# Kernel optimization log

Hardware: AMD Instinct MI355X
Metric: run time of the kernel (lower is better)

Reference implementation:

```python
import jax, jax.numpy as jnp
import numpy as np

B, D = 128, 512
ORDER, DEPTH = 1, 2


def setup_inputs() -> dict:
    key = jax.random.key(0)
    kx, kw = jax.random.split(key)
    x = jax.random.normal(kx, (B, D), dtype=jnp.float32)
    # scale the cubic meta-weight so repeated contractions stay O(1)
    W = jax.random.normal(kw, (D, D, D), dtype=jnp.float32) * (1.0 / np.sqrt(D))
    bias = jnp.zeros((D,), dtype=jnp.float32)
    return {"x": x, "W": W, "bias": bias}


def reference(x, W, bias):
    # Meta-linear: per-sample effective weight obtained by contracting the
    # trailing `ORDER` modes of W (out, in, in, ...) with x, rescaled by
    # 1/sqrt(d) per contraction, then applied as a linear layer; repeat DEPTH times.
    sqrt_d = np.sqrt(x.shape[-1]).astype(np.float32)
    for _ in range(DEPTH):
        # first contraction introduces the batch dim: (out, in, k) x (b, k) -> (b, out, in)
        w = jnp.einsum('...k,bk->b...', W, x) / sqrt_d
        for _ in range(ORDER - 1):
            w = jnp.einsum('b...k,bk->b...', w, x) / sqrt_d
        x = jnp.einsum('boi,bi->bo', w, x) + bias
    return x
```

## Files before the change

kernel.cpp:

```cpp
#include <hip/hip_runtime.h>
#include <hip/hip_fp16.h>


typedef __attribute__((ext_vector_type(8))) _Float16 f16x8;
typedef __attribute__((ext_vector_type(4))) float    f32x4v;
typedef __attribute__((ext_vector_type(4))) unsigned u32x4;

#define DD 512
#define BB 128
#define INV_SQRT_D 0.04419417382415922f

static __device__ __forceinline__ unsigned pkh(float a, float b) {
    __half2 h = __float22half2_rn(make_float2(a, b));
    unsigned u; __builtin_memcpy(&u, &h, sizeof(u)); return u;
}
static __device__ __forceinline__ u32x4 pack8(f32x4v a, f32x4v b) {
    u32x4 r; r.x = pkh(a.x, a.y); r.y = pkh(a.z, a.w);
             r.z = pkh(b.x, b.y); r.w = pkh(b.z, b.w); return r;
}
static __device__ __forceinline__ f16x8 as_h8(u32x4 q) {
    f16x8 v; __builtin_memcpy(&v, &q, sizeof(v)); return v;
}

__global__ __launch_bounds__(256, 4)
void metagemm(const float* __restrict__ x, const float* __restrict__ W,
              float* __restrict__ part) {
    __shared__ u32x4    kp_lds[1024];
    __shared__ unsigned sc_lds[4096];

    const int tid  = threadIdx.x;
    const int lane = tid & 63;
    const int wv   = tid >> 6;
    const int bid  = blockIdx.x;
    const int ob   = bid >> 7;
    const int ig   = (bid >> 3) & 15;
    const int kp   = bid & 7;

    const int o0   = ob * 64 + wv * 16;
    const int i0   = ig * 32;
    const int kb   = kp * 64;
    const int l15  = lane & 15;
    const int quad = lane >> 4;
    const int koff = quad * 8;

    const float* wbase = W + (long)(o0 + l15) * (DD * DD) + (long)i0 * DD + kb + koff;

    f32x4v wa = *(const f32x4v*)(wbase);
    f32x4v wb = *(const f32x4v*)(wbase + 4);
    f32x4v wc = *(const f32x4v*)(wbase + 32);
    f32x4v wd = *(const f32x4v*)(wbase + 36);

#pragma unroll
    for (int ff = 0; ff < 2; ++ff) {
        const int f   = wv * 2 + ff;
        const int row = f * 16 + l15;
        const float* xr = x + row * DD + kb + koff;
#pragma unroll
        for (int ks = 0; ks < 2; ++ks) {
            f32x4v a = *(const f32x4v*)(xr + ks * 32);
            f32x4v b = *(const f32x4v*)(xr + ks * 32 + 4);
            kp_lds[(ks * 8 + f) * 64 + lane] = pack8(a, b);
        }
    }
    {
        const int row  = tid & 127;
        const int half = tid >> 7;
#pragma unroll
        for (int c4 = 0; c4 < 4; ++c4) {
            const int i = half * 16 + c4 * 4;
            f32x4v v = *(const f32x4v*)(x + row * DD + i0 + i);
#pragma unroll
            for (int j = 0; j < 4; ++j) {
                float s = v[j] * INV_SQRT_D;
                sc_lds[(i + j) * 128 + row] = pkh(s, s);
            }
        }
    }
    __syncthreads();

    f32x4v c[8];
#pragma unroll
    for (int f = 0; f < 8; ++f) c[f] = (f32x4v){0.f, 0.f, 0.f, 0.f};

    unsigned lic = 0;
#pragma unroll 1
    for (int n = 0; n < 32; ++n) {
        asm volatile("" : "+v"(lic));

        f32x4v ca = wa, cb = wb, cc = wc, cd = wd;
        if (n < 31) {
            const float* wp = wbase + (n + 1) * DD;
            wa = *(const f32x4v*)(wp);
            wb = *(const f32x4v*)(wp + 4);
            wc = *(const f32x4v*)(wp + 32);
            wd = *(const f32x4v*)(wp + 36);
        }

        f16x8 bf0 = as_h8(pack8(ca, cb));
        f16x8 bf1 = as_h8(pack8(cc, cd));

        const unsigned* scp = sc_lds + n * 128 + l15 + lic;
        const u32x4*    kpp = kp_lds + lane + lic;

#pragma unroll
        for (int f = 0; f < 8; ++f) {
            unsigned su = scp[f * 16];
            u32x4 sq = {su, su, su, su};
            f16x8 sv = as_h8(sq);
            f16x8 a0 = as_h8(kpp[f * 64]) * sv;
            c[f] = __builtin_amdgcn_mfma_f32_16x16x32_f16(a0, bf0, c[f], 0, 0, 0);
            f16x8 a1 = as_h8(kpp[(8 + f) * 64]) * sv;
            c[f] = __builtin_amdgcn_mfma_f32_16x16x32_f16(a1, bf1, c[f], 0, 0, 0);
        }
    }

    float* pbase = part + (long)(ig * 8 + kp) * (BB * DD) + ob * 64;
    const int ocol = wv * 16 + l15;
#pragma unroll
    for (int f = 0; f < 8; ++f) {
#pragma unroll
        for (int r = 0; r < 4; ++r) {
            pbase[(f * 16 + quad * 4 + r) * DD + ocol] = c[f][r];
        }
    }
}

__global__ void reduce_bias(const float* __restrict__ part, const float* __restrict__ bias,
                            float* __restrict__ out) {
    const int idx = blockIdx.x * 256 + threadIdx.x;
    float s = bias[idx & (DD - 1)];
#pragma unroll 16
    for (int p = 0; p < 128; ++p) s += part[(long)p * (BB * DD) + idx];
    out[idx] = s;
}

extern "C" void kernel_launch(void* const* d_in, const int* in_sizes, int n_in,
                              void* d_out, int out_size, void* d_ws, size_t ws_size,
                              hipStream_t stream) {
    (void)in_sizes; (void)n_in; (void)out_size; (void)ws_size;

    const float* x    = (const float*)d_in[0];
    const float* W    = (const float*)d_in[1];
    const float* bias = (const float*)d_in[2];
    float* out = (float*)d_out;

    float* part = (float*)d_ws;
    float* x1   = part + 128 * BB * DD;

    metagemm<<<1024, 256, 0, stream>>>(x, W, part);
    reduce_bias<<<(BB * DD) / 256, 256, 0, stream>>>(part, bias, x1);

    metagemm<<<1024, 256, 0, stream>>>(x1, W, part);
    reduce_bias<<<(BB * DD) / 256, 256, 0, stream>>>(part, bias, out);
}
```

Before: 833.8 us.

## Coalesce W loads via per-wave LDS transpose and deepen prefetch to two rows

Each wave now loads W with lanes covering 16 consecutive float4s of a row across four output rows, giving fully coalesced 256-byte segments. The data is converted to fp16 and staged through a swizzled per-wave LDS buffer to rebuild the MFMA B-fragment layout. The prefetch distance also goes from one to two iterations. The cost is extra LDS writes and reads plus more registers. There is no explicit wave barrier between the LDS write and read, so correctness relies on in-wave ordering.

Measured after the change: 826.5 us. Within noise of the previous version (-0.9%).

```diff
diff --git a/kernel.cpp b/kernel.cpp
--- a/kernel.cpp
+++ b/kernel.cpp
@@ -4,6 +4,7 @@
 
 typedef __attribute__((ext_vector_type(8))) _Float16 f16x8;
 typedef __attribute__((ext_vector_type(4))) float    f32x4v;
+typedef __attribute__((ext_vector_type(2))) unsigned u32x2;
 typedef __attribute__((ext_vector_type(4))) unsigned u32x4;
 
 #define DD 512
@@ -27,6 +28,7 @@
               float* __restrict__ part) {
     __shared__ u32x4    kp_lds[1024];
     __shared__ unsigned sc_lds[4096];
+    __shared__ u32x2    wt_lds[4][256];
 
     const int tid  = threadIdx.x;
     const int lane = tid & 63;
@@ -41,15 +43,32 @@
     const int kb   = kp * 64;
     const int l15  = lane & 15;
     const int quad = lane >> 4;
+
+    const int lr = lane >> 4;
+    const int lc = lane & 15;
+    const float* wp0 = W + (long)(o0 + 0 + lr) * (DD * DD) + (long)i0 * DD + kb + lc * 4;
+    const float* wp1 = W + (long)(o0 + 4 + lr) * (DD * DD) + (long)i0 * DD + kb + lc * 4;
+    const float* wp2 = W + (long)(o0 + 8 + lr) * (DD * DD) + (long)i0 * DD + kb + lc * 4;
+    const float* wp3 = W + (long)(o0 + 12 + lr) * (DD * DD) + (long)i0 * DD + kb + lc * 4;
+
+    u32x2* wtw0 = &wt_lds[wv][(0 + lr) * 16 + (((lc >> 1) ^ ((0 + lr) & 7)) * 2) + (lc & 1)];
+    u32x2* wtw1 = &wt_lds[wv][(4 + lr) * 16 + (((lc >> 1) ^ ((4 + lr) & 7)) * 2) + (lc & 1)];
+    u32x2* wtw2 = &wt_lds[wv][(8 + lr) * 16 + (((lc >> 1) ^ ((8 + lr) & 7)) * 2) + (lc & 1)];
+    u32x2* wtw3 = &wt_lds[wv][(12 + lr) * 16 + (((lc >> 1) ^ ((12 + lr) & 7)) * 2) + (lc & 1)];
+    const u32x4* wtr = (const u32x4*)&wt_lds[wv][0];
+    const u32x4* wtr0 = wtr + l15 * 8 + ((0 * 4 + quad) ^ (l15 & 7));
+    const u32x4* wtr1 = wtr + l15 * 8 + ((1 * 4 + quad) ^ (l15 & 7));
+
+    f32x4v p0a = *(const f32x4v*)(wp0);
+    f32x4v p0b = *(const f32x4v*)(wp1);
+    f32x4v p0c = *(const f32x4v*)(wp2);
+    f32x4v p0d = *(const f32x4v*)(wp3);
+    f32x4v p1a = *(const f32x4v*)(wp0 + DD);
+    f32x4v p1b = *(const f32x4v*)(wp1 + DD);
+    f32x4v p1c = *(const f32x4v*)(wp2 + DD);
+    f32x4v p1d = *(const f32x4v*)(wp3 + DD);
+
     const int koff = quad * 8;
-
-    const float* wbase = W + (long)(o0 + l15) * (DD * DD) + (long)i0 * DD + kb + koff;
-
-    f32x4v wa = *(const f32x4v*)(wbase);
-    f32x4v wb = *(const f32x4v*)(wbase + 4);
-    f32x4v wc = *(const f32x4v*)(wbase + 32);
-    f32x4v wd = *(const f32x4v*)(wbase + 36);
-
 #pragma unroll
     for (int ff = 0; ff < 2; ++ff) {
         const int f   = wv * 2 + ff;
@@ -87,20 +106,26 @@
     for (int n = 0; n < 32; ++n) {
         asm volatile("" : "+v"(lic));
 
-        f32x4v ca = wa, cb = wb, cc = wc, cd = wd;
-        if (n < 31) {
-            const float* wp = wbase + (n + 1) * DD;
-            wa = *(const f32x4v*)(wp);
-            wb = *(const f32x4v*)(wp + 4);
-            wc = *(const f32x4v*)(wp + 32);
-            wd = *(const f32x4v*)(wp + 36);
+        f32x4v ca = p0a, cb = p0b, cc = p0c, cd = p0d;
+        p0a = p1a; p0b = p1b; p0c = p1c; p0d = p1d;
+        if (n < 30) {
+            const long off = (long)(n + 2) * DD;
+            p1a = *(const f32x4v*)(wp0 + off);
+            p1b = *(const f32x4v*)(wp1 + off);
+            p1c = *(const f32x4v*)(wp2 + off);
+            p1d = *(const f32x4v*)(wp3 + off);
         }
 
-        f16x8 bf0 = as_h8(pack8(ca, cb));
-        f16x8 bf1 = as_h8(pack8(cc, cd));
+        *wtw0 = (u32x2){pkh(ca.x, ca.y), pkh(ca.z, ca.w)};
+        *wtw1 = (u32x2){pkh(cb.x, cb.y), pkh(cb.z, cb.w)};
+        *wtw2 = (u32x2){pkh(cc.x, cc.y), pkh(cc.z, cc.w)};
+        *wtw3 = (u32x2){pkh(cd.x, cd.y), pkh(cd.z, cd.w)};
 
         const unsigned* scp = sc_lds + n * 128 + l15 + lic;
         const u32x4*    kpp = kp_lds + lane + lic;
+
+        f16x8 bf0 = as_h8(wtr0[lic]);
+        f16x8 bf1 = as_h8(wtr1[lic]);
 
 #pragma unroll
         for (int f = 0; f < 8; ++f) {
```
